# Kernel optimization log

Measured on AMD Instinct MI355X. Metric: run time of the kernel, lower is better.

The kernel has to match this reference:

```python
import jax, jax.numpy as jnp
import numpy as np

N_EMB = 100000
REPR = 512
BATCH = 8192
HIST = 50
DROP_P = 0.2  # fraction of positions set to -1 sentinel


def setup_inputs() -> dict:
    key = jax.random.key(0)
    k_idx, k_drop, k_w = jax.random.split(key, 3)
    target = jax.random.randint(k_idx, (BATCH, HIST), 0, N_EMB, dtype=jnp.int64)
    drop = jax.random.uniform(k_drop, (BATCH, HIST)) < DROP_P
    drop = drop.at[:, 0].set(False)  # guarantee >=1 valid token per row
    target = jnp.where(drop, jnp.int64(-1), target)
    emb_weight = jax.random.normal(k_w, (N_EMB, REPR), dtype=jnp.float32)
    return {"target": target, "emb_weight": emb_weight}


def reference(target, emb_weight):
    # mask of valid (non -1) positions: [B, L]
    mask = (target != -1)
    safe_idx = jnp.where(mask, target, 0)
    # gather: [B, L, D], zero out sentinel rows, sum over L
    gathered = emb_weight[safe_idx] * mask[..., None].astype(emb_weight.dtype)
    pooled = gathered.sum(axis=1)  # [B, D]
    # original returns [B, 1, D] (each per-token emb is [1, D])
    return pooled[:, None, :]
```

## Files before the change

### kernel.cpp

```cpp
#include <hip/hip_runtime.h>

#define BATCH  8192
#define HIST   50
#define REPR   512
#define N_EMB  100000
#define NSLICE 8
#define SLICE_SZ ((N_EMB + NSLICE - 1) / NSLICE)
#define CH     8

typedef float v4f __attribute__((ext_vector_type(4)));

__global__ __launch_bounds__(256) void embbag_sliced_kernel(
    const int* __restrict__ target,
    const float* __restrict__ emb,
    float* __restrict__ out)
{
    __shared__ int s_idx[2][NSLICE][HIST];
    __shared__ int s_cnt[2][NSLICE];

    const int g    = threadIdx.x >> 7;
    const int lane = threadIdx.x & 127;
    const int row  = blockIdx.x * 2 + g;

    if (lane < NSLICE) s_cnt[g][lane] = 0;
    __syncthreads();
    if (lane < HIST) {
        const int ix = target[row * HIST + lane];
        if (ix >= 0) {
            const int b   = ix / SLICE_SZ;
            const int pos = atomicAdd(&s_cnt[g][b], 1);
            s_idx[g][b][pos] = ix;
        }
    }
    __syncthreads();

    const float* col = emb + (size_t)lane * 4;
    float4 acc = make_float4(0.f, 0.f, 0.f, 0.f);

    for (int p = 0; p < NSLICE; ++p) {
        const int n = s_cnt[g][p];
        for (int k0 = 0; k0 < n; k0 += CH) {
            int    idx[CH];
            float  w[CH];
            float4 v[CH];
#pragma unroll
            for (int k = 0; k < CH; ++k) {
                const bool valid = (k0 + k) < n;
                idx[k] = valid ? s_idx[g][p][k0 + k] : 0;
                w[k]   = valid ? 1.0f : 0.0f;
            }
#pragma unroll
            for (int k = 0; k < CH; ++k) {
                v[k] = *reinterpret_cast<const float4*>(col + (size_t)idx[k] * REPR);
            }
#pragma unroll
            for (int k = 0; k < CH; ++k) {
                acc.x = fmaf(v[k].x, w[k], acc.x);
                acc.y = fmaf(v[k].y, w[k], acc.y);
                acc.z = fmaf(v[k].z, w[k], acc.z);
                acc.w = fmaf(v[k].w, w[k], acc.w);
            }
        }
    }

    v4f av;
    av.x = acc.x; av.y = acc.y; av.z = acc.z; av.w = acc.w;
    v4f* o = reinterpret_cast<v4f*>(out + (size_t)row * REPR + (size_t)lane * 4);
    __builtin_nontemporal_store(av, o);
}

extern "C" void kernel_launch(void* const* d_in, const int* in_sizes, int n_in,
                              void* d_out, int out_size, void* d_ws, size_t ws_size,
                              hipStream_t stream) {
    const int*   target = (const int*)d_in[0];
    const float* emb    = (const float*)d_in[1];
    float*       out    = (float*)d_out;

    dim3 grid(BATCH / 2);
    dim3 block(256);
    embbag_sliced_kernel<<<grid, block, 0, stream>>>(target, emb, out);
}
```

Measured before the change: 100.1 us.

## Phase embedding gathers by table slice with grid-wide barriers for L2 locality

Switches to a persistent-style grid of 1024 blocks, each handling 8 rows. All blocks walk the embedding table in 4 slices and synchronize between slices through global atomic counters, so the working set of each phase is a quarter of the table and can stay resident in L2/MALL. This adds grid-wide spin barriers (with a spin limit) and a counter-reset launch, and it relies on all 1024 blocks being co-resident. If they are not, correctness is still preserved but the blocks fall back to timed-out spinning.

```diff
diff --git a/kernel.cpp b/kernel.cpp
--- a/kernel.cpp
+++ b/kernel.cpp
@@ -1,82 +1,120 @@
 #include <hip/hip_runtime.h>
 
-#define BATCH  8192
-#define HIST   50
-#define REPR   512
-#define N_EMB  100000
-#define NSLICE 8
+#define BATCH   8192
+#define HIST    50
+#define REPR    512
+#define N_EMB   100000
+#define NSLICE  4
 #define SLICE_SZ ((N_EMB + NSLICE - 1) / NSLICE)
-#define CH     8
+#define NBLK    1024
+#define ROWS_PB (BATCH / NBLK)
+#define CH      8
+#define SPIN_LIMIT (1u << 16)
 
 typedef float v4f __attribute__((ext_vector_type(4)));
 
-__global__ __launch_bounds__(256) void embbag_sliced_kernel(
+__global__ void init_counters_kernel(unsigned int* cnt) {
+    if (threadIdx.x < NSLICE) cnt[threadIdx.x] = 0u;
+}
+
+__global__ __launch_bounds__(256, 4) void embbag_phased_kernel(
     const int* __restrict__ target,
     const float* __restrict__ emb,
-    float* __restrict__ out)
+    float* __restrict__ out,
+    unsigned int* __restrict__ cnt)
 {
-    __shared__ int s_idx[2][NSLICE][HIST];
-    __shared__ int s_cnt[2][NSLICE];
+    __shared__ int s_idx[ROWS_PB][NSLICE][HIST + 2];
+    __shared__ int s_cnt[ROWS_PB][NSLICE];
 
     const int g    = threadIdx.x >> 7;
     const int lane = threadIdx.x & 127;
-    const int row  = blockIdx.x * 2 + g;
+    const int base = blockIdx.x * ROWS_PB;
 
-    if (lane < NSLICE) s_cnt[g][lane] = 0;
+    if (threadIdx.x < ROWS_PB * NSLICE)
+        s_cnt[threadIdx.x >> 2][threadIdx.x & 3] = 0;
     __syncthreads();
-    if (lane < HIST) {
-        const int ix = target[row * HIST + lane];
+    for (int t = threadIdx.x; t < ROWS_PB * HIST; t += 256) {
+        const int r  = t / HIST;
+        const int j  = t - r * HIST;
+        const int ix = target[(base + r) * HIST + j];
         if (ix >= 0) {
             const int b   = ix / SLICE_SZ;
-            const int pos = atomicAdd(&s_cnt[g][b], 1);
-            s_idx[g][b][pos] = ix;
+            const int pos = atomicAdd(&s_cnt[r][b], 1);
+            s_idx[r][b][pos] = ix;
         }
     }
     __syncthreads();
 
     const float* col = emb + (size_t)lane * 4;
-    float4 acc = make_float4(0.f, 0.f, 0.f, 0.f);
+    float4 acc[ROWS_PB / 2];
+#pragma unroll
+    for (int c = 0; c < ROWS_PB / 2; ++c)
+        acc[c] = make_float4(0.f, 0.f, 0.f, 0.f);
 
     for (int p = 0; p < NSLICE; ++p) {
-        const int n = s_cnt[g][p];
-        for (int k0 = 0; k0 < n; k0 += CH) {
-            int    idx[CH];
-            float  w[CH];
-            float4 v[CH];
 #pragma unroll
-            for (int k = 0; k < CH; ++k) {
-                const bool valid = (k0 + k) < n;
-                idx[k] = valid ? s_idx[g][p][k0 + k] : 0;
-                w[k]   = valid ? 1.0f : 0.0f;
+        for (int c = 0; c < ROWS_PB / 2; ++c) {
+            const int r = c * 2 + g;
+            const int n = s_cnt[r][p];
+            for (int k0 = 0; k0 < n; k0 += CH) {
+                int    idx[CH];
+                float  w[CH];
+                float4 v[CH];
+#pragma unroll
+                for (int k = 0; k < CH; ++k) {
+                    const bool valid = (k0 + k) < n;
+                    idx[k] = valid ? s_idx[r][p][k0 + k] : 0;
+                    w[k]   = valid ? 1.0f : 0.0f;
+                }
+#pragma unroll
+                for (int k = 0; k < CH; ++k) {
+                    v[k] = *reinterpret_cast<const float4*>(col + (size_t)idx[k] * REPR);
+                }
+#pragma unroll
+                for (int k = 0; k < CH; ++k) {
+                    acc[c].x = fmaf(v[k].x, w[k], acc[c].x);
+                    acc[c].y = fmaf(v[k].y, w[k], acc[c].y);
+                    acc[c].z = fmaf(v[k].z, w[k], acc[c].z);
+                    acc[c].w = fmaf(v[k].w, w[k], acc[c].w);
+                }
             }
-#pragma unroll
-            for (int k = 0; k < CH; ++k) {
-                v[k] = *reinterpret_cast<const float4*>(col + (size_t)idx[k] * REPR);
+        }
+        if (p < NSLICE - 1) {
+            __syncthreads();
+            if (threadIdx.x == 0) {
+                __hip_atomic_fetch_add(&cnt[p], 1u, __ATOMIC_RELAXED,
+                                       __HIP_MEMORY_SCOPE_AGENT);
+                unsigned int spins = 0;
+                while (__hip_atomic_load(&cnt[p], __ATOMIC_RELAXED,
+                                         __HIP_MEMORY_SCOPE_AGENT) < NBLK &&
+                       spins < SPIN_LIMIT) {
+                    ++spins;
+                    __builtin_amdgcn_s_sleep(2);
+                }
             }
-#pragma unroll
-            for (int k = 0; k < CH; ++k) {
-                acc.x = fmaf(v[k].x, w[k], acc.x);
-                acc.y = fmaf(v[k].y, w[k], acc.y);
-                acc.z = fmaf(v[k].z, w[k], acc.z);
-                acc.w = fmaf(v[k].w, w[k], acc.w);
-            }
+            __syncthreads();
         }
     }
 
-    v4f av;
-    av.x = acc.x; av.y = acc.y; av.z = acc.z; av.w = acc.w;
-    v4f* o = reinterpret_cast<v4f*>(out + (size_t)row * REPR + (size_t)lane * 4);
-    __builtin_nontemporal_store(av, o);
+#pragma unroll
+    for (int c = 0; c < ROWS_PB / 2; ++c) {
+        const int row = base + c * 2 + g;
+        v4f av;
+        av.x = acc[c].x; av.y = acc[c].y; av.z = acc[c].z; av.w = acc[c].w;
+        v4f* o = reinterpret_cast<v4f*>(out + (size_t)row * REPR + (size_t)lane * 4);
+        __builtin_nontemporal_store(av, o);
+    }
 }
 
 extern "C" void kernel_launch(void* const* d_in, const int* in_sizes, int n_in,
                               void* d_out, int out_size, void* d_ws, size_t ws_size,
                               hipStream_t stream) {
-    const int*   target = (const int*)d_in[0];
-    const float* emb    = (const float*)d_in[1];
-    float*       out    = (float*)d_out;
+    const int*    target = (const int*)d_in[0];
+    const float*  emb    = (const float*)d_in[1];
+    float*        out    = (float*)d_out;
+    unsigned int* cnt    = (unsigned int*)d_ws;
 
-    dim3 grid(BATCH / 2);
-    dim3 block(256);
-    embbag_sliced_kernel<<<grid, block, 0, stream>>>(target, emb, out);
+    init_counters_kernel<<<1, 64, 0, stream>>>(cnt);
+    embbag_phased_kernel<<<dim3(NBLK), dim3(256), 0, stream>>>(
+        target, emb, out, cnt);
 }
```

After: 324.8 us. 3.24x slower.
